# Optimization experiments

Measured on AMD Instinct MI355X. Metric: run time of the kernel, lower is better.

The kernel has to match this reference:

```python
import jax, jax.numpy as jnp
import numpy as np

NO, NTRAIN, DIM, OUT, K = 8192, 100000, 256, 256, 16


def _conv1d(x, w, b, pad):
    # x: [N, Cin, L], w: [Cout, Cin, ks]
    y = jax.lax.conv_general_dilated(x, w, (1,), [(pad, pad)],
                                     dimension_numbers=("NCH", "OIH", "NCH"))
    return y + b[None, :, None]


def _dist2sim(d):
    inv = 1.0 / (d + 1e-8)
    return inv / jnp.sum(inv, axis=1, keepdims=True)


def setup_inputs() -> dict:
    key = jax.random.key(0)
    ks = jax.random.split(key, 20)
    s = 0.05
    return {
        "X": jax.random.normal(ks[0], (NO, DIM), jnp.float32),
        "X_train": jax.random.normal(ks[1], (NTRAIN, DIM), jnp.float32),
        "y_train": jax.random.normal(ks[2], (NTRAIN,), jnp.float32),
        "neigh_dist": jax.random.uniform(ks[3], (NO, K), jnp.float32, 0.1, 2.0),
        "data_m_train": (jax.random.uniform(ks[4], (NTRAIN, DIM)) > 0.2).astype(jnp.float32),
        "data_m_batch": (jax.random.uniform(ks[5], (NO, DIM)) > 0.2).astype(jnp.float32),
        # attention-layer params (GAT-style)
        "W_att": jax.random.normal(ks[6], (DIM, OUT), jnp.float32) * s,
        "a_src": jax.random.normal(ks[7], (OUT,), jnp.float32) * s,
        "a_dst": jax.random.normal(ks[8], (OUT,), jnp.float32) * s,
        # MLP params (stored as [in, out])
        "w1": jax.random.normal(ks[9], (4 * DIM + 1, 2 * OUT), jnp.float32) * s,
        "b1": jnp.zeros((2 * OUT,), jnp.float32),
        "w2": jax.random.normal(ks[10], (2 * OUT, OUT), jnp.float32) * s,
        "b2": jnp.zeros((OUT,), jnp.float32),
        "w3": jax.random.normal(ks[11], (OUT, 1), jnp.float32) * s,
        "b3": jnp.zeros((1,), jnp.float32),
        # conv params
        "conv1_w": jax.random.normal(ks[12], (1, 1, 3), jnp.float32) * s,
        "conv1_b": jnp.zeros((1,), jnp.float32),
        "convk_w": jax.random.normal(ks[13], (K, K, 5), jnp.float32) * s,
        "convk_b": jnp.zeros((K,), jnp.float32),
        "neigh_ind": jax.random.randint(ks[14], (NO, K), 0, NTRAIN),
    }


def reference(X, X_train, y_train, neigh_dist, data_m_train, data_m_batch,
              W_att, a_src, a_dst, w1, b1, w2, b2, w3, b3,
              conv1_w, conv1_b, convk_w, convk_b, neigh_ind):
    no, dim = X.shape
    k = neigh_ind.shape[1]
    # KNN gather, masked by training missingness mask
    Candidate = X_train[neigh_ind] * data_m_train[neigh_ind]   # [no, k, dim]
    # GAT-style attention (AttentionLayer surrogate); Candidate/dist pass through
    Xm = X * data_m_batch
    h_x = (Xm @ W_att) @ a_src                                  # [no]
    h_c = jnp.einsum("nkd,do->nko", Candidate, W_att) @ a_dst   # [no, k]
    e = jax.nn.leaky_relu(h_x[:, None] + h_c, 0.2)
    a = jax.nn.softmax(e, axis=1)
    b = e
    # distance -> similarity weights, weighted label prediction
    weights = _dist2sim(neigh_dist)                             # [no, k]
    pred = jnp.sum(y_train[neigh_ind] * weights, axis=1)        # [no]
    # distance-weighted neighbor features
    Neighbors_o = Candidate * weights[:, :, None]               # [no, k, dim]
    Neighbors = jnp.max(_conv1d(Neighbors_o, convk_w, convk_b, 2), axis=1)  # [no, dim]
    X1 = _conv1d(X[:, None, :], conv1_w, conv1_b, 1)[:, 0, :]   # [no, dim]
    X2 = jnp.broadcast_to(X[:, None, :], (no, k, dim))
    Inter = jnp.concatenate([X2, Neighbors_o], axis=2)          # [no, k, 2*dim]
    Inter = jnp.max(_conv1d(Inter, convk_w, convk_b, 2), axis=1)  # [no, 2*dim]
    inputs = jnp.concatenate([pred[:, None], X1, Inter, Neighbors], axis=1)  # [no, 4*dim+1]
    # 3-layer MLP (eval mode: dropout off)
    x1 = inputs @ w1 + b1
    x2 = jax.nn.relu(x1 @ w2 + b2)
    x3 = jax.nn.relu((x2 @ w3 + b3)[:, 0])
    return pred + x3, a, b
```

## Files before the change

### kernel.cpp

```cpp
#include <hip/hip_runtime.h>

#define NO 8192
#define NTRAIN 100000
#define DIM 256
#define KNN 16
#define ROWS 8
#define KPAD 1088

#define WS_VSRC 0
#define WS_VDST 256
#define WS_B12  512
#define WS_WCONV 768
#define WS_WSUM 2048
#define WS_KB   2128
#define WS_C1W  2144
#define WS_C1B  2147
#define WS_WB   2176
#define WS_W12  4096
#define WS_W12T 270336
#define WS_PRED 409600
#define WS_INBF 417792
#define WS_END  (417792 + 4456448)
#define WS_NEED_BYTES ((size_t)WS_END * 4)

typedef unsigned int u32;
typedef unsigned short u16;
typedef __attribute__((ext_vector_type(8))) short bf16x8;
typedef __attribute__((ext_vector_type(4))) float f32x4;

__device__ __forceinline__ u16 f2bf(float f){
  u32 u = __float_as_uint(f);
  u32 r = (u + 0x7FFFu + ((u>>16)&1u)) >> 16;
  return (u16)r;
}
__device__ __forceinline__ float bf2f(u16 v){ return __uint_as_float(((u32)v)<<16); }

__global__ __launch_bounds__(256) void k0_prep(
    const float* __restrict__ Watt, const float* __restrict__ asrc, const float* __restrict__ adst,
    const float* __restrict__ b1, const float* __restrict__ w2, const float* __restrict__ b2,
    const float* __restrict__ c1w, const float* __restrict__ c1b,
    const float* __restrict__ ckw, const float* __restrict__ ckb,
    float* __restrict__ ws){
  int tid = threadIdx.x;
  int b = blockIdx.x;
  if (b < 2){
    __shared__ float a_sh[256];
    const float* av = (b==0) ? asrc : adst;
    a_sh[tid] = av[tid];
    __syncthreads();
    const float4* wp = (const float4*)(Watt + tid*DIM);
    float s = 0.f;
    for (int i=0;i<DIM/4;i++){
      float4 u = wp[i];
      int o = i*4;
      s += u.x*a_sh[o+0] + u.y*a_sh[o+1] + u.z*a_sh[o+2] + u.w*a_sh[o+3];
    }
    ws[(b==0?WS_VSRC:WS_VDST) + tid] = s;
  } else if (b == 2){
    float s = b2[tid];
    for (int h=0; h<512; ++h) s += b1[h] * w2[h*256+tid];
    ws[WS_B12+tid] = s;
  } else {
    for (int idx=tid; idx<1280; idx+=256){
      int co = idx/80, r = idx%80; int ci = r/5, t = r%5;
      ws[WS_WCONV + (ci*5+t)*16 + co] = ckw[idx];
    }
    {
      u16* wb = (u16*)(ws + WS_WB);
      for (int e = tid; e < 1536; e += 256){
        int s = e >> 9, rem = e & 511, lane = rem >> 3, j = rem & 7;
        int g = lane >> 4, n = lane & 15;
        int ci = 8*(g&1) + j, t = 2*s + (g>>1);
        float v = (t < 5) ? ckw[n*80 + ci*5 + t] : 0.f;
        wb[e] = f2bf(v);
      }
    }
    __syncthreads();
    if (tid < 80){
      int t = tid/16, co = tid%16;
      float s = 0.f;
      for (int ci=0;ci<16;ci++) s += ws[WS_WCONV + (ci*5+t)*16 + co];
      ws[WS_WSUM + t*16 + co] = s;
    }
    if (tid < 16) ws[WS_KB + tid] = ckb[tid];
    if (tid < 3)  ws[WS_C1W + tid] = c1w[tid];
    if (tid == 3) ws[WS_C1B] = c1b[0];
  }
}

__global__ __launch_bounds__(256) void k1_fold(
    const float* __restrict__ w1, const float* __restrict__ w2, float* __restrict__ ws){
  __shared__ float aT[16][20];
  __shared__ float t16[16][257];
  float* w12 = ws + WS_W12;
  u16* w12t = (u16*)(ws + WS_W12T);
  int tid = threadIdx.x;
  int r0 = blockIdx.x * 16;
  float acc[16];
  #pragma unroll
  for (int j=0;j<16;j++) acc[j] = 0.f;
  int kk = tid & 15, rr = tid >> 4;
  for (int kt=0; kt<32; ++kt){
    int row = r0 + rr;
    float av = (row < 1025) ? w1[row*512 + kt*16 + kk] : 0.f;
    __syncthreads();
    aT[kk][rr] = av;
    __syncthreads();
    #pragma unroll
    for (int k=0;k<16;++k){
      float bv = w2[(kt*16+k)*256 + tid];
      const float* a = aT[k];
      #pragma unroll
      for (int j=0;j<16;j++) acc[j] = fmaf(a[j], bv, acc[j]);
    }
  }
  #pragma unroll
  for (int j=0;j<16;j++){
    int row = r0 + j;
    if (row < 1040) w12[(size_t)row*256 + tid] = (row < 1025) ? acc[j] : 0.f;
    t16[j][tid] = (row < 1025) ? acc[j] : 0.f;
  }
  __syncthreads();
  for (int p=0; p<16; ++p){
    int nn = p*16 + (tid>>4);
    int kl = tid & 15;
    w12t[(size_t)nn*KPAD + r0 + kl] = f2bf(t16[kl][nn]);
  }
}

__global__ __launch_bounds__(256) void k2a_stage(
    const float* __restrict__ X, const float* __restrict__ Xtr, const float* __restrict__ ytr,
    const float* __restrict__ ndist, const float* __restrict__ mtr, const float* __restrict__ mb,
    const int* __restrict__ nind,
    float* __restrict__ ws,
    float* __restrict__ outA, float* __restrict__ outB){
  __shared__ float x_sh[256];
  __shared__ __align__(16) short candT[262][24];
  __shared__ float nm_sh[256];
  __shared__ float corr_sh[10][16];
  __shared__ float wgt_sh[16];
  __shared__ int   idx_sh[16];
  __shared__ float red_sh[4];
  __shared__ float hx_sh, pred_sh;
  __shared__ float hc_sh[16];

  int n = blockIdx.x;
  int tid = threadIdx.x;
  const float* vsrc = ws + WS_VSRC;
  const float* vdst = ws + WS_VDST;
  const float* wcv  = ws + WS_WCONV;
  const float* wsum = ws + WS_WSUM;
  const float* kb   = ws + WS_KB;
  u16* inbf = (u16*)(ws + WS_INBF) + (size_t)n*KPAD;

  float xv = X[n*256+tid];
  x_sh[tid] = xv;
  float part = xv * mb[n*256+tid] * vsrc[tid];
  #pragma unroll
  for (int off=32; off; off>>=1) part += __shfl_xor(part, off, 64);
  if ((tid&63)==0) red_sh[tid>>6] = part;
  if (tid<16){
    int j = nind[n*16+tid];
    idx_sh[tid] = j;
    float d = ndist[n*16+tid];
    float inv = 1.f/(d + 1e-8f);
    float s = inv;
    #pragma unroll
    for (int off=8; off; off>>=1) s += __shfl_xor(s, off, 16);
    float w = inv/s;
    wgt_sh[tid] = w;
    float pp = ytr[j] * w;
    #pragma unroll
    for (int off=8; off; off>>=1) pp += __shfl_xor(pp, off, 16);
    if (tid==0) pred_sh = pp;
  }
  __syncthreads();

  if (tid==0) hx_sh = red_sh[0]+red_sh[1]+red_sh[2]+red_sh[3];
  {
    u32* dst = (u32*)&candT[2+tid][0];
    #pragma unroll
    for (int q=0;q<8;q++){
      int i0 = idx_sh[2*q]*256 + tid;
      int i1 = idx_sh[2*q+1]*256 + tid;
      float v0 = Xtr[i0]*mtr[i0]*wgt_sh[2*q];
      float v1 = Xtr[i1]*mtr[i1]*wgt_sh[2*q+1];
      dst[q] = (u32)f2bf(v0) | ((u32)f2bf(v1) << 16);
    }
  }
  if (tid < 6){
    int r = (tid < 2) ? tid : 256 + tid;
    u32* dst = (u32*)&candT[r][0];
    #pragma unroll
    for (int q=0;q<12;q++) dst[q] = 0;
  }
  __syncthreads();

  {
    int k = tid>>4, d0 = tid&15;
    float s = 0.f;
    #pragma unroll
    for (int i=0;i<16;i++){
      int d = d0 + i*16;
      s += bf2f((u16)candT[2+d][k]) * vdst[d];
    }
    #pragma unroll
    for (int off=8; off; off>>=1) s += __shfl_xor(s, off, 16);
    if (d0==0) hc_sh[k] = s / wgt_sh[k];
  }
  if (tid < 160){
    const int tt[10] = {4,3,4,2,3,4,1,2,3,4};
    const int pp[10] = {0,0,1,0,1,2,0,1,2,3};
    int pair = tid >> 4, co = tid & 15;
    int t = tt[pair], p = pp[pair];
    float s = 0.f;
    #pragma unroll
    for (int ci=0; ci<16; ++ci)
      s += wcv[(ci*5+t)*16+co] * bf2f((u16)candT[2+p][ci]);
    corr_sh[pair][co] = s;
  }
  float im1;
  {
    float a2[16];
    #pragma unroll
    for (int j=0;j<16;j++) a2[j] = kb[j];
    #pragma unroll
    for (int t=0;t<5;++t){
      int pos = tid + t - 2;
      float v = x_sh[pos & 255];
      v = (pos >= 0 && pos < 256) ? v : 0.f;
      const float* wb_ = wsum + t*16;
      #pragma unroll
      for (int j=0;j<16;j++) a2[j] = fmaf(v, wb_[j], a2[j]);
    }
    im1 = a2[0];
    #pragma unroll
    for (int j=1;j<16;j++) im1 = fmaxf(im1, a2[j]);
  }
  float x1v = ws[WS_C1B];
  #pragma unroll
  for (int t=0;t<3;++t){
    int pos = tid + t - 1;
    float v = x_sh[pos & 255];
    v = (pos>=0 && pos<256) ? v : 0.f;
    x1v = fmaf(v, ws[WS_C1W+t], x1v);
  }
  {
    int lane = tid & 63, wave = tid >> 6;
    int g    = lane >> 4;
    int lm   = lane & 15;
    int colh = g & 1;
    int tg   = g >> 1;
    const u16* wb = (const u16*)(ws + WS_WB);
    bf16x8 bfr0 = *(const bf16x8*)(wb + 0*512 + lane*8);
    bf16x8 bfr1 = *(const bf16x8*)(wb + 1*512 + lane*8);
    bf16x8 bfr2 = *(const bf16x8*)(wb + 2*512 + lane*8);
    float kbv = kb[lm];
    #pragma unroll
    for (int i=0;i<4;i++){
      int m0 = (wave*4 + i) * 16;
      f32x4 a = {kbv, kbv, kbv, kbv};
      int rbase = m0 + lm + tg;
      bf16x8 af0 = *(const bf16x8*)&candT[rbase + 0][8*colh];
      a = __builtin_amdgcn_mfma_f32_16x16x32_bf16(af0, bfr0, a, 0,0,0);
      bf16x8 af1 = *(const bf16x8*)&candT[rbase + 2][8*colh];
      a = __builtin_amdgcn_mfma_f32_16x16x32_bf16(af1, bfr1, a, 0,0,0);
      bf16x8 af2 = *(const bf16x8*)&candT[rbase + 4][8*colh];
      a = __builtin_amdgcn_mfma_f32_16x16x32_bf16(af2, bfr2, a, 0,0,0);
      #pragma unroll
      for (int off=1; off<16; off<<=1){
        #pragma unroll
        for (int r=0;r<4;r++){
          float o = __shfl_xor(a[r], off, 64);
          a[r] = fmaxf(a[r], o);
        }
      }
      if (lm == 0){
        float4 st; st.x=a[0]; st.y=a[1]; st.z=a[2]; st.w=a[3];
        *(float4*)&nm_sh[m0 + g*4] = st;
      }
    }
  }
  __syncthreads();

  if (tid<16){
    float e = hx_sh + hc_sh[tid];
    e = (e>=0.f) ? e : 0.2f*e;
    outB[n*16+tid] = e;
    float m = e;
    #pragma unroll
    for (int off=8; off; off>>=1) m = fmaxf(m, __shfl_xor(m, off, 16));
    float ex = __expf(e - m);
    float ssum = ex;
    #pragma unroll
    for (int off=8; off; off>>=1) ssum += __shfl_xor(ssum, off, 16);
    outA[n*16+tid] = ex/ssum;
  }
  float nm = nm_sh[tid];
  if (tid >= 254){
    float a2[16];
    #pragma unroll
    for (int j=0;j<16;j++) a2[j] = kb[j];
    #pragma unroll
    for (int t=0;t<5;++t){
      int pos = tid + t - 2;
      float v = (pos < 256) ? x_sh[pos] : 0.f;
      const float* wb_ = wsum + t*16;
      #pragma unroll
      for (int j=0;j<16;j++) a2[j] = fmaf(v, wb_[j], a2[j]);
    }
    if (tid == 254){
      #pragma unroll
      for (int j=0;j<16;j++) a2[j] += corr_sh[0][j];
    } else {
      #pragma unroll
      for (int j=0;j<16;j++) a2[j] += corr_sh[1][j] + corr_sh[2][j];
    }
    im1 = a2[0];
    #pragma unroll
    for (int j=1;j<16;j++) im1 = fmaxf(im1, a2[j]);
  }
  float im2 = nm;
  if (tid < 2){
    float a3[16];
    if (tid == 0){
      #pragma unroll
      for (int j=0;j<16;j++)
        a3[j] = kb[j] + wsum[0*16+j]*x_sh[254] + wsum[1*16+j]*x_sh[255]
              + corr_sh[3][j] + corr_sh[4][j] + corr_sh[5][j];
    } else {
      #pragma unroll
      for (int j=0;j<16;j++)
        a3[j] = kb[j] + wsum[0*16+j]*x_sh[255]
              + corr_sh[6][j] + corr_sh[7][j] + corr_sh[8][j] + corr_sh[9][j];
    }
    im2 = a3[0];
    #pragma unroll
    for (int j=1;j<16;j++) im2 = fmaxf(im2, a3[j]);
  }

  inbf[1 + tid]   = f2bf(x1v);
  inbf[257 + tid] = f2bf(im1);
  inbf[513 + tid] = f2bf(im2);
  inbf[769 + tid] = f2bf(nm);
  if (tid == 0){ inbf[0] = f2bf(pred_sh); ws[WS_PRED + n] = pred_sh; }
  if (tid < 63) inbf[1025 + tid] = 0;
}

__global__ __launch_bounds__(256) void k2b_mlp(
    const float* __restrict__ ws, const float* __restrict__ w3, const float* __restrict__ b3,
    float* __restrict__ out0){
  __shared__ __align__(16) u16 A_sh[32][72];
  __shared__ __align__(16) u16 B_sh[256][72];
  __shared__ float pr[32][2];
  int tid = threadIdx.x;
  int r0 = blockIdx.x * 32;
  const u16* inbf = (const u16*)(ws + WS_INBF);
  const u16* w12t = (const u16*)(ws + WS_W12T);
  int lane = tid & 63, wv = tid >> 6;
  int lm = lane & 15, g = lane >> 4;
  int mt = wv & 1, nh = wv >> 1;
  f32x4 acc[8];
  #pragma unroll
  for (int q=0;q<8;q++){
    float b = ws[WS_B12 + (nh*8+q)*16 + lm];
    acc[q][0]=b; acc[q][1]=b; acc[q][2]=b; acc[q][3]=b;
  }
  int arow = tid >> 3, ak0 = (tid & 7)*8;
  const u16* asrc_p = inbf + (size_t)(r0+arow)*KPAD + ak0;
  const u16* bsrc_p = w12t + (size_t)tid*KPAD;
  for (int kt=0; kt<17; ++kt){
    __syncthreads();
    *(bf16x8*)&A_sh[arow][ak0] = *(const bf16x8*)(asrc_p + kt*64);
    #pragma unroll
    for (int j=0;j<8;j++)
      *(bf16x8*)&B_sh[tid][8*j] = *(const bf16x8*)(bsrc_p + kt*64 + 8*j);
    __syncthreads();
    #pragma unroll
    for (int ks=0; ks<2; ++ks){
      bf16x8 af = *(const bf16x8*)&A_sh[mt*16+lm][ks*32 + g*8];
      #pragma unroll
      for (int q=0;q<8;q++){
        bf16x8 bf_ = *(const bf16x8*)&B_sh[(nh*8+q)*16+lm][ks*32 + g*8];
        acc[q] = __builtin_amdgcn_mfma_f32_16x16x32_bf16(af, bf_, acc[q], 0,0,0);
      }
    }
  }
  float w3v[8];
  #pragma unroll
  for (int q=0;q<8;q++) w3v[q] = w3[(nh*8+q)*16 + lm];
  #pragma unroll
  for (int j=0;j<4;j++){
    float p = 0.f;
    #pragma unroll
    for (int q=0;q<8;q++) p += fmaxf(acc[q][j], 0.f) * w3v[q];
    #pragma unroll
    for (int off=1; off<16; off<<=1) p += __shfl_xor(p, off, 64);
    if (lm == 0) pr[mt*16 + g*4 + j][nh] = p;
  }
  __syncthreads();
  if (tid < 32){
    float s = pr[tid][0] + pr[tid][1] + b3[0];
    out0[r0 + tid] = ws[WS_PRED + r0 + tid] + fmaxf(s, 0.f);
  }
}

__global__ __launch_bounds__(256) void k2_fused(
    const float* __restrict__ X, const float* __restrict__ Xtr, const float* __restrict__ ytr,
    const float* __restrict__ ndist, const float* __restrict__ mtr, const float* __restrict__ mb,
    const int* __restrict__ nind,
    const float* __restrict__ ws,
    const float* __restrict__ w3, const float* __restrict__ b3,
    float* __restrict__ out0, float* __restrict__ outA, float* __restrict__ outB){
  __shared__ float x_sh[256];
  __shared__ float cand_sh[16][256];
  __shared__ __align__(16) float in_sh[ROWS][1028];
  __shared__ float corr_sh[10][16];
  __shared__ float wgt_sh[16];
  __shared__ int   idx_sh[16];
  __shared__ float red_sh[ROWS][4];
  __shared__ float hx_sh;
  __shared__ float pred_s[ROWS];
  __shared__ float hc_sh[16];

  int n0 = blockIdx.x * ROWS;
  int tid = threadIdx.x;
  const float* vsrc = ws + WS_VSRC;
  const float* vdst = ws + WS_VDST;
  const float* wcv  = ws + WS_WCONV;
  const float* wsum = ws + WS_WSUM;
  const float* kb   = ws + WS_KB;

  for (int r = 0; r < ROWS; ++r){
    int n = n0 + r;
    __syncthreads();
    float xv = X[n*256+tid];
    x_sh[tid] = xv;
    float xm = xv * mb[n*256+tid];
    float part = xm * vsrc[tid];
    #pragma unroll
    for (int off=32; off; off>>=1) part += __shfl_xor(part, off, 64);
    if ((tid&63)==0) red_sh[0][tid>>6] = part;
    __syncthreads();
    if (tid==0) hx_sh = red_sh[0][0]+red_sh[0][1]+red_sh[0][2]+red_sh[0][3];
    if (tid<16){
      int j = nind[n*16+tid];
      idx_sh[tid] = j;
      float d = ndist[n*16+tid];
      float inv = 1.f/(d + 1e-8f);
      float s = inv;
      #pragma unroll
      for (int off=8; off; off>>=1) s += __shfl_xor(s, off, 16);
      float w = inv/s;
      wgt_sh[tid] = w;
      float pp = ytr[j] * w;
      #pragma unroll
      for (int off=8; off; off>>=1) pp += __shfl_xor(pp, off, 16);
      if (tid==0){ pred_s[r] = pp; in_sh[r][0] = pp; }
    }
    __syncthreads();
    {
      int kk4 = tid >> 6;
      int c4 = (tid & 63) * 4;
      #pragma unroll
      for (int g=0; g<4; ++g){
        int k = g*4 + kk4;
        size_t basei = (size_t)idx_sh[k]*256 + c4;
        float4 xv4 = *(const float4*)(Xtr + basei);
        float4 mv4 = *(const float4*)(mtr + basei);
        float4 cv;
        cv.x = xv4.x*mv4.x; cv.y = xv4.y*mv4.y; cv.z = xv4.z*mv4.z; cv.w = xv4.w*mv4.w;
        *(float4*)&cand_sh[k][c4] = cv;
      }
    }
    __syncthreads();
    {
      int k = tid>>4, d0 = tid&15;
      float s = 0.f;
      #pragma unroll
      for (int i=0;i<16;i++){ int d = d0 + i*16; s += cand_sh[k][d]*vdst[d]; }
      #pragma unroll
      for (int off=8; off; off>>=1) s += __shfl_xor(s, off, 16);
      if (d0==0) hc_sh[k] = s;
    }
    __syncthreads();
    if (tid<16){
      float e = hx_sh + hc_sh[tid];
      e = (e>=0.f) ? e : 0.2f*e;
      outB[n*16+tid] = e;
      float m = e;
      #pragma unroll
      for (int off=8; off; off>>=1) m = fmaxf(m, __shfl_xor(m, off, 16));
      float ex = __expf(e - m);
      float ssum = ex;
      #pragma unroll
      for (int off=8; off; off>>=1) ssum += __shfl_xor(ssum, off, 16);
      outA[n*16+tid] = ex/ssum;
    }
    #pragma unroll
    for (int k=0;k<16;k++) cand_sh[k][tid] *= wgt_sh[k];
    __syncthreads();
    if (tid < 160){
      const int tt[10] = {4,3,4,2,3,4,1,2,3,4};
      const int pp[10] = {0,0,1,0,1,2,0,1,2,3};
      int pair = tid >> 4, co = tid & 15;
      int t = tt[pair], p = pp[pair];
      float s = 0.f;
      #pragma unroll
      for (int ci=0; ci<16; ++ci) s += wcv[(ci*5+t)*16+co] * cand_sh[ci][p];
      corr_sh[pair][co] = s;
    }
    float acc[16];
    #pragma unroll
    for (int j=0;j<16;j++) acc[j] = kb[j];
    for (int ci=0; ci<16; ++ci){
      const float* wci = wcv + ci*80;
      #pragma unroll
      for (int t=0;t<5;++t){
        int pos = tid + t - 2;
        float v = cand_sh[ci][pos & 255];
        v = (pos >= 0 && pos < 256) ? v : 0.f;
        const float* wb_ = wci + t*16;
        #pragma unroll
        for (int j=0;j<16;j++) acc[j] = fmaf(v, wb_[j], acc[j]);
      }
    }
    float nm = acc[0];
    #pragma unroll
    for (int j=1;j<16;j++) nm = fmaxf(nm, acc[j]);
    float a2[16];
    #pragma unroll
    for (int j=0;j<16;j++) a2[j] = kb[j];
    #pragma unroll
    for (int t=0;t<5;++t){
      int pos = tid + t - 2;
      float v = x_sh[pos & 255];
      v = (pos >= 0 && pos < 256) ? v : 0.f;
      const float* wb_ = wsum + t*16;
      #pragma unroll
      for (int j=0;j<16;j++) a2[j] = fmaf(v, wb_[j], a2[j]);
    }
    __syncthreads();
    if (tid == 254){
      #pragma unroll
      for (int j=0;j<16;j++) a2[j] += corr_sh[0][j];
    }
    if (tid == 255){
      #pragma unroll
      for (int j=0;j<16;j++) a2[j] += corr_sh[1][j] + corr_sh[2][j];
    }
    float im1 = a2[0];
    #pragma unroll
    for (int j=1;j<16;j++) im1 = fmaxf(im1, a2[j]);
    float im2 = nm;
    if (tid < 2){
      float a3[16];
      if (tid == 0){
        #pragma unroll
        for (int j=0;j<16;j++)
          a3[j] = kb[j] + wsum[0*16+j]*x_sh[254] + wsum[1*16+j]*x_sh[255]
                + corr_sh[3][j] + corr_sh[4][j] + corr_sh[5][j];
      } else {
        #pragma unroll
        for (int j=0;j<16;j++)
          a3[j] = kb[j] + wsum[0*16+j]*x_sh[255]
                + corr_sh[6][j] + corr_sh[7][j] + corr_sh[8][j] + corr_sh[9][j];
      }
      im2 = a3[0];
      #pragma unroll
      for (int j=1;j<16;j++) im2 = fmaxf(im2, a3[j]);
    }
    float x1v = ws[WS_C1B];
    #pragma unroll
    for (int t=0;t<3;++t){
      int pos = tid + t - 1;
      float v = x_sh[pos & 255];
      v = (pos>=0 && pos<256) ? v : 0.f;
      x1v = fmaf(v, ws[WS_C1W+t], x1v);
    }
    in_sh[r][1 + tid]   = x1v;
    in_sh[r][257 + tid] = im1;
    in_sh[r][513 + tid] = im2;
    in_sh[r][769 + tid] = nm;
  }
  __syncthreads();
  const float* W12 = ws + WS_W12;
  float b12v = ws[WS_B12 + tid];
  float z[ROWS];
  #pragma unroll
  for (int r=0;r<ROWS;r++) z[r] = b12v;
  for (int c=0; c<1024; c+=4){
    float w0 = W12[(size_t)(c+0)*256 + tid];
    float w1v = W12[(size_t)(c+1)*256 + tid];
    float w2v = W12[(size_t)(c+2)*256 + tid];
    float w3v_ = W12[(size_t)(c+3)*256 + tid];
    #pragma unroll
    for (int r=0;r<ROWS;r++){
      float4 iv = *(const float4*)&in_sh[r][c];
      z[r] = fmaf(iv.x, w0, z[r]);
      z[r] = fmaf(iv.y, w1v, z[r]);
      z[r] = fmaf(iv.z, w2v, z[r]);
      z[r] = fmaf(iv.w, w3v_, z[r]);
    }
  }
  {
    float wl = W12[(size_t)1024*256 + tid];
    #pragma unroll
    for (int r=0;r<ROWS;r++) z[r] = fmaf(in_sh[r][1024], wl, z[r]);
  }
  float w3v = w3[tid];
  #pragma unroll
  for (int r=0;r<ROWS;r++){
    float p = fmaxf(z[r], 0.f) * w3v;
    #pragma unroll
    for (int off=32; off; off>>=1) p += __shfl_xor(p, off, 64);
    if ((tid&63)==0) red_sh[r][tid>>6] = p;
  }
  __syncthreads();
  if (tid < ROWS){
    float s = red_sh[tid][0]+red_sh[tid][1]+red_sh[tid][2]+red_sh[tid][3] + b3[0];
    float x3 = fmaxf(s, 0.f);
    out0[n0 + tid] = pred_s[tid] + x3;
  }
}

extern "C" void kernel_launch(void* const* d_in, const int* in_sizes, int n_in,
                              void* d_out, int out_size, void* d_ws, size_t ws_size,
                              hipStream_t stream){
  const float* X    = (const float*)d_in[0];
  const float* Xtr  = (const float*)d_in[1];
  const float* ytr  = (const float*)d_in[2];
  const float* nd   = (const float*)d_in[3];
  const float* mtr  = (const float*)d_in[4];
  const float* mb   = (const float*)d_in[5];
  const float* Watt = (const float*)d_in[6];
  const float* asrc = (const float*)d_in[7];
  const float* adst = (const float*)d_in[8];
  const float* w1   = (const float*)d_in[9];
  const float* b1   = (const float*)d_in[10];
  const float* w2   = (const float*)d_in[11];
  const float* b2   = (const float*)d_in[12];
  const float* w3   = (const float*)d_in[13];
  const float* b3   = (const float*)d_in[14];
  const float* c1w  = (const float*)d_in[15];
  const float* c1b  = (const float*)d_in[16];
  const float* ckw  = (const float*)d_in[17];
  const float* ckb  = (const float*)d_in[18];
  const int* nind = (const int*)d_in[19];
  float* ws = (float*)d_ws;
  float* out0 = (float*)d_out;
  float* outA = out0 + NO;
  float* outB = out0 + NO + NO*KNN;

  k0_prep<<<dim3(4), dim3(256), 0, stream>>>(Watt, asrc, adst, b1, w2, b2, c1w, c1b, ckw, ckb, ws);
  k1_fold<<<dim3(68), dim3(256), 0, stream>>>(w1, w2, ws);
  if (ws_size >= WS_NEED_BYTES){
    k2a_stage<<<dim3(NO), dim3(256), 0, stream>>>(X, Xtr, ytr, nd, mtr, mb, nind,
                                                  ws, outA, outB);
    k2b_mlp<<<dim3(NO/32), dim3(256), 0, stream>>>((const float*)ws, w3, b3, out0);
  } else {
    k2_fused<<<dim3(NO/ROWS), dim3(256), 0, stream>>>(X, Xtr, ytr, nd, mtr, mb, nind,
                                                      (const float*)ws, w3, b3,
                                                      out0, outA, outB);
  }
}
```

Measured before the change: 155.3 us.

## Merge prep kernels, remove barrier in staging, swap MFMA operands, prefetch MLP tiles

Merges k0_prep into k1_fold as four extra blocks, removing one kernel launch. In k2a_stage, neighbour indices and weights are now computed redundantly in every 16-lane group and broadcast with shuffles, which drops a block-wide barrier before the gather. The conv MFMA operands are swapped so the max reduction over channels needs only two cross-lane shuffles instead of a 16-step butterfly. The MLP GEMM prefetches the next A/B tile into registers while the current tile is being consumed, at the cost of higher register pressure.

```diff
diff --git a/kernel.cpp b/kernel.cpp
--- a/kernel.cpp
+++ b/kernel.cpp
@@ -35,66 +35,65 @@
 }
 __device__ __forceinline__ float bf2f(u16 v){ return __uint_as_float(((u32)v)<<16); }
 
-__global__ __launch_bounds__(256) void k0_prep(
+__global__ __launch_bounds__(256) void k1_fold(
+    const float* __restrict__ w1, const float* __restrict__ w2,
     const float* __restrict__ Watt, const float* __restrict__ asrc, const float* __restrict__ adst,
-    const float* __restrict__ b1, const float* __restrict__ w2, const float* __restrict__ b2,
+    const float* __restrict__ b1, const float* __restrict__ b2,
     const float* __restrict__ c1w, const float* __restrict__ c1b,
     const float* __restrict__ ckw, const float* __restrict__ ckb,
     float* __restrict__ ws){
   int tid = threadIdx.x;
-  int b = blockIdx.x;
-  if (b < 2){
-    __shared__ float a_sh[256];
-    const float* av = (b==0) ? asrc : adst;
-    a_sh[tid] = av[tid];
-    __syncthreads();
-    const float4* wp = (const float4*)(Watt + tid*DIM);
-    float s = 0.f;
-    for (int i=0;i<DIM/4;i++){
-      float4 u = wp[i];
-      int o = i*4;
-      s += u.x*a_sh[o+0] + u.y*a_sh[o+1] + u.z*a_sh[o+2] + u.w*a_sh[o+3];
-    }
-    ws[(b==0?WS_VSRC:WS_VDST) + tid] = s;
-  } else if (b == 2){
-    float s = b2[tid];
-    for (int h=0; h<512; ++h) s += b1[h] * w2[h*256+tid];
-    ws[WS_B12+tid] = s;
-  } else {
-    for (int idx=tid; idx<1280; idx+=256){
-      int co = idx/80, r = idx%80; int ci = r/5, t = r%5;
-      ws[WS_WCONV + (ci*5+t)*16 + co] = ckw[idx];
-    }
-    {
-      u16* wb = (u16*)(ws + WS_WB);
-      for (int e = tid; e < 1536; e += 256){
-        int s = e >> 9, rem = e & 511, lane = rem >> 3, j = rem & 7;
-        int g = lane >> 4, n = lane & 15;
-        int ci = 8*(g&1) + j, t = 2*s + (g>>1);
-        float v = (t < 5) ? ckw[n*80 + ci*5 + t] : 0.f;
-        wb[e] = f2bf(v);
-      }
-    }
-    __syncthreads();
-    if (tid < 80){
-      int t = tid/16, co = tid%16;
+  if (blockIdx.x >= 68){
+    int b = blockIdx.x - 68;
+    if (b < 2){
+      __shared__ float a_sh[256];
+      const float* av = (b==0) ? asrc : adst;
+      a_sh[tid] = av[tid];
+      __syncthreads();
+      const float4* wp = (const float4*)(Watt + tid*DIM);
       float s = 0.f;
-      for (int ci=0;ci<16;ci++) s += ws[WS_WCONV + (ci*5+t)*16 + co];
-      ws[WS_WSUM + t*16 + co] = s;
-    }
-    if (tid < 16) ws[WS_KB + tid] = ckb[tid];
-    if (tid < 3)  ws[WS_C1W + tid] = c1w[tid];
-    if (tid == 3) ws[WS_C1B] = c1b[0];
-  }
-}
-
-__global__ __launch_bounds__(256) void k1_fold(
-    const float* __restrict__ w1, const float* __restrict__ w2, float* __restrict__ ws){
+      for (int i=0;i<DIM/4;i++){
+        float4 u = wp[i];
+        int o = i*4;
+        s += u.x*a_sh[o+0] + u.y*a_sh[o+1] + u.z*a_sh[o+2] + u.w*a_sh[o+3];
+      }
+      ws[(b==0?WS_VSRC:WS_VDST) + tid] = s;
+    } else if (b == 2){
+      float s = b2[tid];
+      for (int h=0; h<512; ++h) s += b1[h] * w2[h*256+tid];
+      ws[WS_B12+tid] = s;
+    } else {
+      for (int idx=tid; idx<1280; idx+=256){
+        int co = idx/80, r = idx%80; int ci = r/5, t = r%5;
+        ws[WS_WCONV + (ci*5+t)*16 + co] = ckw[idx];
+      }
+      {
+        u16* wb = (u16*)(ws + WS_WB);
+        for (int e = tid; e < 1536; e += 256){
+          int s = e >> 9, rem = e & 511, lane = rem >> 3, j = rem & 7;
+          int g = lane >> 4, nn = lane & 15;
+          int ci = 8*(g&1) + j, t = 2*s + (g>>1);
+          float v = (t < 5) ? ckw[nn*80 + ci*5 + t] : 0.f;
+          wb[e] = f2bf(v);
+        }
+      }
+      __syncthreads();
+      if (tid < 80){
+        int t = tid/16, co = tid%16;
+        float s = 0.f;
+        for (int ci=0;ci<16;ci++) s += ws[WS_WCONV + (ci*5+t)*16 + co];
+        ws[WS_WSUM + t*16 + co] = s;
+      }
+      if (tid < 16) ws[WS_KB + tid] = ckb[tid];
+      if (tid < 3)  ws[WS_C1W + tid] = c1w[tid];
+      if (tid == 3) ws[WS_C1B] = c1b[0];
+    }
+    return;
+  }
   __shared__ float aT[16][20];
   __shared__ float t16[16][257];
   float* w12 = ws + WS_W12;
   u16* w12t = (u16*)(ws + WS_W12T);
-  int tid = threadIdx.x;
   int r0 = blockIdx.x * 16;
   float acc[16];
   #pragma unroll
@@ -138,11 +137,9 @@
   __shared__ __align__(16) short candT[262][24];
   __shared__ float nm_sh[256];
   __shared__ float corr_sh[10][16];
-  __shared__ float wgt_sh[16];
-  __shared__ int   idx_sh[16];
   __shared__ float red_sh[4];
-  __shared__ float hx_sh, pred_sh;
   __shared__ float hc_sh[16];
+  __shared__ float pred_sh;
 
   int n = blockIdx.x;
   int tid = threadIdx.x;
@@ -153,46 +150,44 @@
   const float* kb   = ws + WS_KB;
   u16* inbf = (u16*)(ws + WS_INBF) + (size_t)n*KPAD;
 
+  int l16 = tid & 15;
+  int j16 = nind[n*16 + l16];
+  float d16 = ndist[n*16 + l16];
+  float inv = 1.f/(d16 + 1e-8f);
+  float ssum = inv;
+  #pragma unroll
+  for (int off=8; off; off>>=1) ssum += __shfl_xor(ssum, off, 16);
+  float w16 = inv / ssum;
+
+  {
+    u32* dst = (u32*)&candT[2+tid][0];
+    #pragma unroll
+    for (int q=0;q<8;q++){
+      int ja = __shfl(j16, 2*q, 16), jb = __shfl(j16, 2*q+1, 16);
+      float wa = __shfl(w16, 2*q, 16), wb2 = __shfl(w16, 2*q+1, 16);
+      int ia = ja*256 + tid, ib = jb*256 + tid;
+      float va = Xtr[ia]*mtr[ia]*wa;
+      float vb = Xtr[ib]*mtr[ib]*wb2;
+      dst[q] = (u32)f2bf(va) | ((u32)f2bf(vb) << 16);
+    }
+  }
+  if (tid < 6){
+    int r = (tid < 2) ? tid : 256 + tid;
+    u32* dst = (u32*)&candT[r][0];
+    #pragma unroll
+    for (int q=0;q<12;q++) dst[q] = 0;
+  }
   float xv = X[n*256+tid];
   x_sh[tid] = xv;
   float part = xv * mb[n*256+tid] * vsrc[tid];
   #pragma unroll
   for (int off=32; off; off>>=1) part += __shfl_xor(part, off, 64);
   if ((tid&63)==0) red_sh[tid>>6] = part;
-  if (tid<16){
-    int j = nind[n*16+tid];
-    idx_sh[tid] = j;
-    float d = ndist[n*16+tid];
-    float inv = 1.f/(d + 1e-8f);
-    float s = inv;
-    #pragma unroll
-    for (int off=8; off; off>>=1) s += __shfl_xor(s, off, 16);
-    float w = inv/s;
-    wgt_sh[tid] = w;
-    float pp = ytr[j] * w;
+  if (tid < 16){
+    float pp = ytr[j16] * w16;
     #pragma unroll
     for (int off=8; off; off>>=1) pp += __shfl_xor(pp, off, 16);
     if (tid==0) pred_sh = pp;
-  }
-  __syncthreads();
-
-  if (tid==0) hx_sh = red_sh[0]+red_sh[1]+red_sh[2]+red_sh[3];
-  {
-    u32* dst = (u32*)&candT[2+tid][0];
-    #pragma unroll
-    for (int q=0;q<8;q++){
-      int i0 = idx_sh[2*q]*256 + tid;
-      int i1 = idx_sh[2*q+1]*256 + tid;
-      float v0 = Xtr[i0]*mtr[i0]*wgt_sh[2*q];
-      float v1 = Xtr[i1]*mtr[i1]*wgt_sh[2*q+1];
-      dst[q] = (u32)f2bf(v0) | ((u32)f2bf(v1) << 16);
-    }
-  }
-  if (tid < 6){
-    int r = (tid < 2) ? tid : 256 + tid;
-    u32* dst = (u32*)&candT[r][0];
-    #pragma unroll
-    for (int q=0;q<12;q++) dst[q] = 0;
   }
   __syncthreads();
 
@@ -206,7 +201,8 @@
     }
     #pragma unroll
     for (int off=8; off; off>>=1) s += __shfl_xor(s, off, 16);
-    if (d0==0) hc_sh[k] = s / wgt_sh[k];
+    float wk = __shfl(w16, k, 16);
+    if (d0==0) hc_sh[k] = s / wk;
   }
   if (tid < 160){
     const int tt[10] = {4,3,4,2,3,4,1,2,3,4};
@@ -252,49 +248,42 @@
     int colh = g & 1;
     int tg   = g >> 1;
     const u16* wb = (const u16*)(ws + WS_WB);
-    bf16x8 bfr0 = *(const bf16x8*)(wb + 0*512 + lane*8);
-    bf16x8 bfr1 = *(const bf16x8*)(wb + 1*512 + lane*8);
-    bf16x8 bfr2 = *(const bf16x8*)(wb + 2*512 + lane*8);
-    float kbv = kb[lm];
+    bf16x8 wfr0 = *(const bf16x8*)(wb + 0*512 + lane*8);
+    bf16x8 wfr1 = *(const bf16x8*)(wb + 1*512 + lane*8);
+    bf16x8 wfr2 = *(const bf16x8*)(wb + 2*512 + lane*8);
+    float4 kb4 = *(const float4*)&kb[g*4];
     #pragma unroll
     for (int i=0;i<4;i++){
       int m0 = (wave*4 + i) * 16;
-      f32x4 a = {kbv, kbv, kbv, kbv};
+      f32x4 a = {kb4.x, kb4.y, kb4.z, kb4.w};
       int rbase = m0 + lm + tg;
-      bf16x8 af0 = *(const bf16x8*)&candT[rbase + 0][8*colh];
-      a = __builtin_amdgcn_mfma_f32_16x16x32_bf16(af0, bfr0, a, 0,0,0);
-      bf16x8 af1 = *(const bf16x8*)&candT[rbase + 2][8*colh];
-      a = __builtin_amdgcn_mfma_f32_16x16x32_bf16(af1, bfr1, a, 0,0,0);
-      bf16x8 af2 = *(const bf16x8*)&candT[rbase + 4][8*colh];
-      a = __builtin_amdgcn_mfma_f32_16x16x32_bf16(af2, bfr2, a, 0,0,0);
-      #pragma unroll
-      for (int off=1; off<16; off<<=1){
-        #pragma unroll
-        for (int r=0;r<4;r++){
-          float o = __shfl_xor(a[r], off, 64);
-          a[r] = fmaxf(a[r], o);
-        }
-      }
-      if (lm == 0){
-        float4 st; st.x=a[0]; st.y=a[1]; st.z=a[2]; st.w=a[3];
-        *(float4*)&nm_sh[m0 + g*4] = st;
-      }
+      bf16x8 cf0 = *(const bf16x8*)&candT[rbase + 0][8*colh];
+      a = __builtin_amdgcn_mfma_f32_16x16x32_bf16(wfr0, cf0, a, 0,0,0);
+      bf16x8 cf1 = *(const bf16x8*)&candT[rbase + 2][8*colh];
+      a = __builtin_amdgcn_mfma_f32_16x16x32_bf16(wfr1, cf1, a, 0,0,0);
+      bf16x8 cf2 = *(const bf16x8*)&candT[rbase + 4][8*colh];
+      a = __builtin_amdgcn_mfma_f32_16x16x32_bf16(wfr2, cf2, a, 0,0,0);
+      float mx = fmaxf(fmaxf(a[0], a[1]), fmaxf(a[2], a[3]));
+      mx = fmaxf(mx, __shfl_xor(mx, 16, 64));
+      mx = fmaxf(mx, __shfl_xor(mx, 32, 64));
+      if (g == 0) nm_sh[m0 + lm] = mx;
     }
   }
   __syncthreads();
 
   if (tid<16){
-    float e = hx_sh + hc_sh[tid];
+    float hx = red_sh[0]+red_sh[1]+red_sh[2]+red_sh[3];
+    float e = hx + hc_sh[tid];
     e = (e>=0.f) ? e : 0.2f*e;
     outB[n*16+tid] = e;
     float m = e;
     #pragma unroll
     for (int off=8; off; off>>=1) m = fmaxf(m, __shfl_xor(m, off, 16));
     float ex = __expf(e - m);
-    float ssum = ex;
-    #pragma unroll
-    for (int off=8; off; off>>=1) ssum += __shfl_xor(ssum, off, 16);
-    outA[n*16+tid] = ex/ssum;
+    float s2 = ex;
+    #pragma unroll
+    for (int off=8; off; off>>=1) s2 += __shfl_xor(s2, off, 16);
+    outA[n*16+tid] = ex/s2;
   }
   float nm = nm_sh[tid];
   if (tid >= 254){
@@ -367,15 +356,23 @@
     acc[q][0]=b; acc[q][1]=b; acc[q][2]=b; acc[q][3]=b;
   }
   int arow = tid >> 3, ak0 = (tid & 7)*8;
-  const u16* asrc_p = inbf + (size_t)(r0+arow)*KPAD + ak0;
-  const u16* bsrc_p = w12t + (size_t)tid*KPAD;
+  const u16* ap = inbf + (size_t)(r0+arow)*KPAD + ak0;
+  const u16* bp = w12t + (size_t)tid*KPAD;
+  bf16x8 aR = *(const bf16x8*)ap;
+  bf16x8 bR[8];
+  #pragma unroll
+  for (int j=0;j<8;j++) bR[j] = *(const bf16x8*)(bp + 8*j);
   for (int kt=0; kt<17; ++kt){
-    __syncthreads();
-    *(bf16x8*)&A_sh[arow][ak0] = *(const bf16x8*)(asrc_p + kt*64);
-    #pragma unroll
-    for (int j=0;j<8;j++)
-      *(bf16x8*)&B_sh[tid][8*j] = *(const bf16x8*)(bsrc_p + kt*64 + 8*j);
-    __syncthreads();
+    if (kt) __syncthreads();
+    *(bf16x8*)&A_sh[arow][ak0] = aR;
+    #pragma unroll
+    for (int j=0;j<8;j++) *(bf16x8*)&B_sh[tid][8*j] = bR[j];
+    __syncthreads();
+    if (kt < 16){
+      aR = *(const bf16x8*)(ap + (kt+1)*64);
+      #pragma unroll
+      for (int j=0;j<8;j++) bR[j] = *(const bf16x8*)(bp + (kt+1)*64 + 8*j);
+    }
     #pragma unroll
     for (int ks=0; ks<2; ++ks){
       bf16x8 af = *(const bf16x8*)&A_sh[mt*16+lm][ks*32 + g*8];
@@ -652,8 +649,8 @@
   float* outA = out0 + NO;
   float* outB = out0 + NO + NO*KNN;
 
-  k0_prep<<<dim3(4), dim3(256), 0, stream>>>(Watt, asrc, adst, b1, w2, b2, c1w, c1b, ckw, ckb, ws);
-  k1_fold<<<dim3(68), dim3(256), 0, stream>>>(w1, w2, ws);
+  k1_fold<<<dim3(72), dim3(256), 0, stream>>>(w1, w2, Watt, asrc, adst, b1, b2,
+                                              c1w, c1b, ckw, ckb, ws);
   if (ws_size >= WS_NEED_BYTES){
     k2a_stage<<<dim3(NO), dim3(256), 0, stream>>>(X, Xtr, ytr, nd, mtr, mb, nind,
                                                   ws, outA, outB);
```

After: 138.1 us. 1.12x faster.
